# Kernel tuning notes

Hardware: AMD Instinct MI355X
Metric: run time of the kernel (lower is better)

The kernel has to match this reference:

```python
import jax, jax.numpy as jnp
import numpy as np

T, B, I, H = 128, 256, 512, 1024  # time, batch, input_size, hidden_size


def setup_inputs() -> dict:
    key = jax.random.key(0)
    k1, k2, k3, k4, k5 = jax.random.split(key, 5)
    s = 1.0 / np.sqrt(H)  # matches torch GRUCell uniform(-1/sqrt(H), 1/sqrt(H)) scale
    return {
        "input_seq": jax.random.normal(k1, (T, B, I), dtype=jnp.float32),
        "W_ih": jax.random.uniform(k2, (3 * H, I), minval=-s, maxval=s, dtype=jnp.float32),
        "W_hh": jax.random.uniform(k3, (3 * H, H), minval=-s, maxval=s, dtype=jnp.float32),
        "b_ih": jax.random.uniform(k4, (3 * H,), minval=-s, maxval=s, dtype=jnp.float32),
        "b_hh": jax.random.uniform(k5, (3 * H,), minval=-s, maxval=s, dtype=jnp.float32),
    }


def reference(input_seq, W_ih, W_hh, b_ih, b_hh):
    # Original torch code calls GRUCell(input_seq[i]) with NO hidden state and never
    # feeds the output back, so hx = 0 at EVERY step -> no recurrence; fully vectorizable.
    Hd = W_hh.shape[1]
    # input gates for all timesteps at once: (T, B, 3H)
    gi = jnp.einsum('tbi,gi->tbg', input_seq, W_ih) + b_ih
    # hidden gates with hx = 0: zeros @ W_hh.T + b_hh == b_hh broadcast, shape (B, 3H)
    h0 = jnp.zeros((input_seq.shape[1], Hd), dtype=input_seq.dtype)
    gh = h0 @ W_hh.T + b_hh
    i_r, i_z, i_n = gi[..., :Hd], gi[..., Hd:2 * Hd], gi[..., 2 * Hd:]
    h_r, h_z, h_n = gh[..., :Hd], gh[..., Hd:2 * Hd], gh[..., 2 * Hd:]
    r = jax.nn.sigmoid(i_r + h_r)
    z = jax.nn.sigmoid(i_z + h_z)
    n = jnp.tanh(i_n + r * h_n)
    h = (1.0 - z) * n + z * h0  # z*h0 == 0, kept for faithfulness
    # torch.stack(output, dim=1) -> (B, T, H)
    return jnp.transpose(h, (1, 0, 2))
```

## Files before the change

kernel.cpp:

```cpp
#include <hip/hip_runtime.h>
#include <hip/hip_bf16.h>

using f32x4  = __attribute__((ext_vector_type(4))) float;
using bf16x8 = __attribute__((ext_vector_type(8))) short;
using s16x4  = __attribute__((ext_vector_type(4))) short;

#define TT 128
#define BB 256
#define II 512
#define HH 1024
#define MM (TT * BB)

__device__ __forceinline__ short f2bf(float f) {
    unsigned u = __float_as_uint(f);
    u = u + 0x7FFFu + ((u >> 16) & 1u);
    return (short)(u >> 16);
}

__device__ __forceinline__ float sigmoid_f(float x) {
    float e = __expf(-fabsf(x));
    float s = 1.0f / (1.0f + e);
    return x >= 0.0f ? s : 1.0f - s;
}

__device__ __forceinline__ float tanh_f(float x) {
    float e = __expf(-2.0f * fabsf(x));
    float t = (1.0f - e) / (1.0f + e);
    return x >= 0.0f ? t : -t;
}

__device__ __forceinline__ void gload_lds16(const void* g, void* l) {
    __builtin_amdgcn_global_load_lds((const __attribute__((address_space(1))) unsigned*)g,
                                     (__attribute__((address_space(3))) unsigned*)l,
                                     16, 0, 0);
}

__global__ __launch_bounds__(256)
void cvt_both_kernel(const float* __restrict__ A, const float* __restrict__ W,
                     short* __restrict__ dst, int nA8, int nTot8) {
    const int stride = gridDim.x * blockDim.x;
    for (int i = blockIdx.x * blockDim.x + threadIdx.x; i < nTot8; i += stride) {
        const float* src = (i < nA8) ? (A + (size_t)i * 8) : (W + (size_t)(i - nA8) * 8);
        f32x4 v0 = ((const f32x4*)src)[0];
        f32x4 v1 = ((const f32x4*)src)[1];
        bf16x8 o;
        o[0] = f2bf(v0.x); o[1] = f2bf(v0.y); o[2] = f2bf(v0.z); o[3] = f2bf(v0.w);
        o[4] = f2bf(v1.x); o[5] = f2bf(v1.y); o[6] = f2bf(v1.z); o[7] = f2bf(v1.w);
        ((bf16x8*)dst)[i] = o;
    }
}

__global__ __launch_bounds__(256, 2)
void gru_gemm_db_kernel(const short* __restrict__ Abf,
                        const short* __restrict__ Wbf,
                        const float* __restrict__ bih,
                        const float* __restrict__ bhh,
                        float* __restrict__ out)
{
    __shared__ char lds[81920];

    const int tid  = threadIdx.x;
    const int wid  = tid >> 6;
    const int lane = tid & 63;
    const int l15  = lane & 15;
    const int l4   = lane >> 4;

    const int mtile = blockIdx.x & 255;
    const int htile = blockIdx.x >> 8;
    const int m0 = mtile * 128;
    const int h0 = htile * 64;

    const int lr8 = lane >> 3;
    const int lc  = lane & 7;
    const int csw = (lc * 16) ^ (lr8 << 4);

    const char* Ab = (const char*)Abf;
    const char* Wb = (const char*)Wbf;

    size_t aAddr[4];
    size_t wAddr[6];
    #pragma unroll
    for (int j = 0; j < 4; ++j)
        aAddr[j] = (size_t)(m0 + (wid * 4 + j) * 8 + lr8) * 1024 + csw;
    #pragma unroll
    for (int j = 0; j < 6; ++j) {
        const int row = (wid * 6 + j) * 8 + lr8;
        const int g   = row >> 6;
        const int wr  = row & 63;
        wAddr[j] = (size_t)(g * HH + h0 + wr) * 1024 + csw;
    }

#define STAGE(t, p)                                                           \
    do {                                                                      \
        const int kb_ = (t) * 128;                                            \
        _Pragma("unroll")                                                     \
        for (int j = 0; j < 4; ++j)                                           \
            gload_lds16(Ab + aAddr[j] + kb_,                                  \
                        lds + (p) * 16384 + (wid * 4 + j) * 1024);            \
        _Pragma("unroll")                                                     \
        for (int j = 0; j < 6; ++j)                                           \
            gload_lds16(Wb + wAddr[j] + kb_,                                  \
                        lds + 32768 + (p) * 24576 + (wid * 6 + j) * 1024);    \
    } while (0)

    f32x4 acc[2][12];
    #pragma unroll
    for (int i = 0; i < 2; ++i)
        #pragma unroll
        for (int j = 0; j < 12; ++j)
            acc[i][j] = (f32x4){0.f, 0.f, 0.f, 0.f};

    STAGE(0, 0);

    const int xsw = (l15 & 7) << 4;

    #pragma unroll
    for (int t = 0; t < 8; ++t) {
        const int p = t & 1;
        if (t < 7) {
            STAGE(t + 1, p ^ 1);
            asm volatile("s_waitcnt vmcnt(10)" ::: "memory");
        } else {
            asm volatile("s_waitcnt vmcnt(0)" ::: "memory");
        }
        __builtin_amdgcn_s_barrier();
        __builtin_amdgcn_sched_barrier(0);

        const char* Al = lds + p * 16384;
        const char* Wl = lds + 32768 + p * 24576;

        #pragma unroll
        for (int kk = 0; kk < 2; ++kk) {
            const int cb = kk * 64 + l4 * 16;
            const int r0 = wid * 32 + l15;
            bf16x8 a0 = *(const bf16x8*)(Al + r0 * 128 + (cb ^ xsw));
            bf16x8 a1 = *(const bf16x8*)(Al + (r0 + 16) * 128 + (cb ^ xsw));
            #pragma unroll
            for (int nf = 0; nf < 12; ++nf) {
                const int rn = nf * 16 + l15;
                bf16x8 b = *(const bf16x8*)(Wl + rn * 128 + (cb ^ xsw));
                acc[0][nf] = __builtin_amdgcn_mfma_f32_16x16x32_bf16(a0, b, acc[0][nf], 0, 0, 0);
                acc[1][nf] = __builtin_amdgcn_mfma_f32_16x16x32_bf16(a1, b, acc[1][nf], 0, 0, 0);
            }
        }
        __builtin_amdgcn_sched_barrier(0);
        __builtin_amdgcn_s_barrier();
    }
#undef STAGE

    #pragma unroll
    for (int nf = 0; nf < 4; ++nf) {
        const int h = h0 + nf * 16 + l15;
        const float bir = bih[h]          + bhh[h];
        const float biz = bih[HH + h]     + bhh[HH + h];
        const float bin = bih[2 * HH + h];
        const float bhn = bhh[2 * HH + h];
        #pragma unroll
        for (int mf = 0; mf < 2; ++mf) {
            const f32x4 ra = acc[mf][nf];
            const f32x4 za = acc[mf][nf + 4];
            const f32x4 na = acc[mf][nf + 8];
            #pragma unroll
            for (int j = 0; j < 4; ++j) {
                const int m = m0 + wid * 32 + mf * 16 + l4 * 4 + j;
                const int tt = m >> 8;
                const int bb = m & 255;
                const float r = sigmoid_f(ra[j] + bir);
                const float z = sigmoid_f(za[j] + biz);
                const float n = tanh_f(na[j] + bin + r * bhn);
                out[(size_t)bb * (TT * HH) + (size_t)tt * HH + h] = (1.0f - z) * n;
            }
        }
    }
}

__global__ __launch_bounds__(256, 2)
void gru_fused_kernel(const float* __restrict__ A,
                      const float* __restrict__ Wih,
                      const float* __restrict__ bih,
                      const float* __restrict__ bhh,
                      float* __restrict__ out)
{
    __shared__ short As[128 * 64];
    __shared__ short Ws[192 * 64];

    const int tid  = threadIdx.x;
    const int wid  = tid >> 6;
    const int lane = tid & 63;
    const int l15  = lane & 15;
    const int l4   = lane >> 4;

    const int mtile = blockIdx.x >> 4;
    const int htile = blockIdx.x & 15;
    const int m0 = mtile * 128;
    const int h0 = htile * 64;

    const int rbase = tid >> 4;
    const int c4    = tid & 15;
    const int swz   = (rbase & 7) << 3;

    f32x4 acc[2][12];
    #pragma unroll
    for (int i = 0; i < 2; ++i)
        #pragma unroll
        for (int j = 0; j < 12; ++j)
            acc[i][j] = (f32x4){0.f, 0.f, 0.f, 0.f};

    for (int kt = 0; kt < II / 64; ++kt) {
        const int k0 = kt * 64;
        __syncthreads();
        const float* Abp = A + (size_t)(m0 + rbase) * II + k0 + c4 * 4;
        #pragma unroll
        for (int i = 0; i < 8; ++i) {
            f32x4 v = *(const f32x4*)(Abp + (size_t)i * 16 * II);
            s16x4 hv;
            hv.x = f2bf(v.x); hv.y = f2bf(v.y); hv.z = f2bf(v.z); hv.w = f2bf(v.w);
            *(s16x4*)(As + (i * 16 + rbase) * 64 + ((c4 * 4) ^ swz)) = hv;
        }
        #pragma unroll
        for (int i = 0; i < 12; ++i) {
            const int row = i * 16 + rbase;
            const int g   = row >> 6;
            const int r   = row & 63;
            f32x4 v = *(const f32x4*)(Wih + (size_t)(g * HH + h0 + r) * II + k0 + c4 * 4);
            s16x4 hv;
            hv.x = f2bf(v.x); hv.y = f2bf(v.y); hv.z = f2bf(v.z); hv.w = f2bf(v.w);
            *(s16x4*)(Ws + row * 64 + ((c4 * 4) ^ swz)) = hv;
        }
        __syncthreads();

        #pragma unroll
        for (int kk = 0; kk < 2; ++kk) {
            const int kc = kk * 32 + l4 * 8;
            const int r0 = wid * 32 + l15;
            bf16x8 a0 = *(const bf16x8*)(As + r0 * 64 + (kc ^ ((r0 & 7) << 3)));
            bf16x8 a1 = *(const bf16x8*)(As + (r0 + 16) * 64 + (kc ^ ((r0 & 7) << 3)));
            #pragma unroll
            for (int nf = 0; nf < 12; ++nf) {
                const int rn = nf * 16 + l15;
                bf16x8 b = *(const bf16x8*)(Ws + rn * 64 + (kc ^ ((rn & 7) << 3)));
                acc[0][nf] = __builtin_amdgcn_mfma_f32_16x16x32_bf16(a0, b, acc[0][nf], 0, 0, 0);
                acc[1][nf] = __builtin_amdgcn_mfma_f32_16x16x32_bf16(a1, b, acc[1][nf], 0, 0, 0);
            }
        }
    }

    #pragma unroll
    for (int nf = 0; nf < 4; ++nf) {
        const int h = h0 + nf * 16 + l15;
        const float bir = bih[h]          + bhh[h];
        const float biz = bih[HH + h]     + bhh[HH + h];
        const float bin = bih[2 * HH + h];
        const float bhn = bhh[2 * HH + h];
        #pragma unroll
        for (int mf = 0; mf < 2; ++mf) {
            const f32x4 ra = acc[mf][nf];
            const f32x4 za = acc[mf][nf + 4];
            const f32x4 na = acc[mf][nf + 8];
            #pragma unroll
            for (int j = 0; j < 4; ++j) {
                const int m = m0 + wid * 32 + mf * 16 + l4 * 4 + j;
                const int tt = m >> 8;
                const int bb = m & 255;
                const float r = sigmoid_f(ra[j] + bir);
                const float z = sigmoid_f(za[j] + biz);
                const float n = tanh_f(na[j] + bin + r * bhn);
                out[(size_t)bb * (TT * HH) + (size_t)tt * HH + h] = (1.0f - z) * n;
            }
        }
    }
}

extern "C" void kernel_launch(void* const* d_in, const int* in_sizes, int n_in,
                              void* d_out, int out_size, void* d_ws, size_t ws_size,
                              hipStream_t stream) {
    const float* input = (const float*)d_in[0];
    const float* Wih   = (const float*)d_in[1];
    const float* bih   = (const float*)d_in[3];
    const float* bhh   = (const float*)d_in[4];
    float* out = (float*)d_out;

    const size_t nA = (size_t)MM * II;
    const size_t nW = (size_t)3 * HH * II;
    const size_t need = (nA + nW) * sizeof(short);

    if (ws_size >= need) {
        short* Abf = (short*)d_ws;
        cvt_both_kernel<<<4096, 256, 0, stream>>>(input, Wih, Abf,
                                                  (int)(nA / 8), (int)((nA + nW) / 8));
        const int nblocks = (MM / 128) * (HH / 64);
        gru_gemm_db_kernel<<<nblocks, 256, 0, stream>>>(Abf, Abf + nA, bih, bhh, out);
    } else {
        const int nblocks = (MM / 128) * (HH / 64);
        gru_fused_kernel<<<nblocks, 256, 0, stream>>>(input, Wih, bih, bhh, out);
    }
}
```

Baseline: 338.5 us.

## Split GEMM tile across 8 waves with single-buffered LDS for higher occupancy

The bf16 GEMM+GRU kernel now runs 512 threads (8 waves in a 4x2 M/N grid) per 128x192 tile instead of 4 waves. Each wave holds a quarter of the accumulators, and the double-buffered LDS pipeline becomes a single buffer with syncthreads around each K stage. This halves LDS and registers per wave so more waves fit per CU and latency can be hidden by occupancy. In exchange it drops the explicit load/compute overlap and adds two block-wide barriers per K step.

```diff
diff --git a/kernel.cpp b/kernel.cpp
--- a/kernel.cpp
+++ b/kernel.cpp
@@ -50,20 +50,22 @@
     }
 }
 
-__global__ __launch_bounds__(256, 2)
-void gru_gemm_db_kernel(const short* __restrict__ Abf,
+__global__ __launch_bounds__(512, 4)
+void gru_gemm_w8_kernel(const short* __restrict__ Abf,
                         const short* __restrict__ Wbf,
                         const float* __restrict__ bih,
                         const float* __restrict__ bhh,
                         float* __restrict__ out)
 {
-    __shared__ char lds[81920];
+    __shared__ char lds[40960];
 
     const int tid  = threadIdx.x;
     const int wid  = tid >> 6;
     const int lane = tid & 63;
     const int l15  = lane & 15;
     const int l4   = lane >> 4;
+    const int wm   = wid & 3;
+    const int wn   = wid >> 2;
 
     const int mtile = blockIdx.x & 255;
     const int htile = blockIdx.x >> 8;
@@ -77,92 +79,90 @@
     const char* Ab = (const char*)Abf;
     const char* Wb = (const char*)Wbf;
 
-    size_t aAddr[4];
-    size_t wAddr[6];
-    #pragma unroll
-    for (int j = 0; j < 4; ++j)
-        aAddr[j] = (size_t)(m0 + (wid * 4 + j) * 8 + lr8) * 1024 + csw;
-    #pragma unroll
-    for (int j = 0; j < 6; ++j) {
-        const int row = (wid * 6 + j) * 8 + lr8;
+    size_t aAddr[2];
+    size_t wAddr[3];
+    #pragma unroll
+    for (int j = 0; j < 2; ++j)
+        aAddr[j] = (size_t)(m0 + (wid * 2 + j) * 8 + lr8) * 1024 + csw;
+    #pragma unroll
+    for (int j = 0; j < 3; ++j) {
+        const int row = (wid * 3 + j) * 8 + lr8;
         const int g   = row >> 6;
         const int wr  = row & 63;
         wAddr[j] = (size_t)(g * HH + h0 + wr) * 1024 + csw;
     }
 
-#define STAGE(t, p)                                                           \
+#define STAGE(t)                                                              \
     do {                                                                      \
         const int kb_ = (t) * 128;                                            \
         _Pragma("unroll")                                                     \
-        for (int j = 0; j < 4; ++j)                                           \
-            gload_lds16(Ab + aAddr[j] + kb_,                                  \
-                        lds + (p) * 16384 + (wid * 4 + j) * 1024);            \
+        for (int j = 0; j < 2; ++j)                                           \
+            gload_lds16(Ab + aAddr[j] + kb_, lds + (wid * 2 + j) * 1024);     \
         _Pragma("unroll")                                                     \
-        for (int j = 0; j < 6; ++j)                                           \
+        for (int j = 0; j < 3; ++j)                                           \
             gload_lds16(Wb + wAddr[j] + kb_,                                  \
-                        lds + 32768 + (p) * 24576 + (wid * 6 + j) * 1024);    \
+                        lds + 16384 + (wid * 3 + j) * 1024);                  \
     } while (0)
 
-    f32x4 acc[2][12];
-    #pragma unroll
-    for (int i = 0; i < 2; ++i)
-        #pragma unroll
-        for (int j = 0; j < 12; ++j)
-            acc[i][j] = (f32x4){0.f, 0.f, 0.f, 0.f};
-
-    STAGE(0, 0);
+    f32x4 acc[2][3][2];
+    #pragma unroll
+    for (int mf = 0; mf < 2; ++mf)
+        #pragma unroll
+        for (int g = 0; g < 3; ++g)
+            #pragma unroll
+            for (int nh = 0; nh < 2; ++nh)
+                acc[mf][g][nh] = (f32x4){0.f, 0.f, 0.f, 0.f};
 
     const int xsw = (l15 & 7) << 4;
 
-    #pragma unroll
     for (int t = 0; t < 8; ++t) {
-        const int p = t & 1;
-        if (t < 7) {
-            STAGE(t + 1, p ^ 1);
-            asm volatile("s_waitcnt vmcnt(10)" ::: "memory");
-        } else {
-            asm volatile("s_waitcnt vmcnt(0)" ::: "memory");
-        }
-        __builtin_amdgcn_s_barrier();
-        __builtin_amdgcn_sched_barrier(0);
-
-        const char* Al = lds + p * 16384;
-        const char* Wl = lds + 32768 + p * 24576;
+        __syncthreads();
+        STAGE(t);
+        __syncthreads();
 
         #pragma unroll
         for (int kk = 0; kk < 2; ++kk) {
             const int cb = kk * 64 + l4 * 16;
-            const int r0 = wid * 32 + l15;
-            bf16x8 a0 = *(const bf16x8*)(Al + r0 * 128 + (cb ^ xsw));
-            bf16x8 a1 = *(const bf16x8*)(Al + (r0 + 16) * 128 + (cb ^ xsw));
-            #pragma unroll
-            for (int nf = 0; nf < 12; ++nf) {
-                const int rn = nf * 16 + l15;
-                bf16x8 b = *(const bf16x8*)(Wl + rn * 128 + (cb ^ xsw));
-                acc[0][nf] = __builtin_amdgcn_mfma_f32_16x16x32_bf16(a0, b, acc[0][nf], 0, 0, 0);
-                acc[1][nf] = __builtin_amdgcn_mfma_f32_16x16x32_bf16(a1, b, acc[1][nf], 0, 0, 0);
-            }
-        }
-        __builtin_amdgcn_sched_barrier(0);
-        __builtin_amdgcn_s_barrier();
+            bf16x8 a[2], b[3][2];
+            #pragma unroll
+            for (int mf = 0; mf < 2; ++mf) {
+                const int r = wm * 32 + mf * 16 + l15;
+                a[mf] = *(const bf16x8*)(lds + r * 128 + (cb ^ xsw));
+            }
+            #pragma unroll
+            for (int g = 0; g < 3; ++g)
+                #pragma unroll
+                for (int nh = 0; nh < 2; ++nh) {
+                    const int rn = g * 64 + wn * 32 + nh * 16 + l15;
+                    b[g][nh] = *(const bf16x8*)(lds + 16384 + rn * 128 + (cb ^ xsw));
+                }
+            #pragma unroll
+            for (int mf = 0; mf < 2; ++mf)
+                #pragma unroll
+                for (int g = 0; g < 3; ++g)
+                    #pragma unroll
+                    for (int nh = 0; nh < 2; ++nh)
+                        acc[mf][g][nh] = __builtin_amdgcn_mfma_f32_16x16x32_bf16(
+                            a[mf], b[g][nh], acc[mf][g][nh], 0, 0, 0);
+        }
     }
 #undef STAGE
 
     #pragma unroll
-    for (int nf = 0; nf < 4; ++nf) {
-        const int h = h0 + nf * 16 + l15;
+    for (int nh = 0; nh < 2; ++nh) {
+        const int h = h0 + wn * 32 + nh * 16 + l15;
         const float bir = bih[h]          + bhh[h];
         const float biz = bih[HH + h]     + bhh[HH + h];
         const float bin = bih[2 * HH + h];
         const float bhn = bhh[2 * HH + h];
         #pragma unroll
         for (int mf = 0; mf < 2; ++mf) {
-            const f32x4 ra = acc[mf][nf];
-            const f32x4 za = acc[mf][nf + 4];
-            const f32x4 na = acc[mf][nf + 8];
+            const f32x4 ra = acc[mf][0][nh];
+            const f32x4 za = acc[mf][1][nh];
+            const f32x4 na = acc[mf][2][nh];
             #pragma unroll
             for (int j = 0; j < 4; ++j) {
-                const int m = m0 + wid * 32 + mf * 16 + l4 * 4 + j;
+                const int m = m0 + wm * 32 + mf * 16 + l4 * 4 + j;
                 const int tt = m >> 8;
                 const int bb = m & 255;
                 const float r = sigmoid_f(ra[j] + bir);
@@ -289,7 +289,7 @@
         cvt_both_kernel<<<4096, 256, 0, stream>>>(input, Wih, Abf,
                                                   (int)(nA / 8), (int)((nA + nW) / 8));
         const int nblocks = (MM / 128) * (HH / 64);
-        gru_gemm_db_kernel<<<nblocks, 256, 0, stream>>>(Abf, Abf + nA, bih, bhh, out);
+        gru_gemm_w8_kernel<<<nblocks, 512, 0, stream>>>(Abf, Abf + nA, bih, bhh, out);
     } else {
         const int nblocks = (MM / 128) * (HH / 64);
         gru_fused_kernel<<<nblocks, 256, 0, stream>>>(input, Wih, bih, bhh, out);
```

New measurement: 352.1 us. +4.0%, slower.
